# Performance work log

Hardware: AMD Instinct MI355X
Metric: run time of the kernel (lower is better)

The kernel has to match this reference:

```python
import jax, jax.numpy as jnp
import numpy as np
import math

B, H, S, D = 4, 16, 2048, 64

def setup_inputs() -> dict:
    key = jax.random.key(0)
    kq, kk, kv, km = jax.random.split(key, 4)
    query = jax.random.normal(kq, (B, H, S, D), dtype=jnp.float32)
    k = jax.random.normal(kk, (B, H, S, D), dtype=jnp.float32)
    value = jax.random.normal(kv, (B, H, S, D), dtype=jnp.float32)
    mask = jax.random.randint(km, (1, 1, S, S), 0, 2) == 1  # True = masked
    return {"query": query, "key": k, "value": value, "mask": mask}

def reference(query, key, value, mask):
    # scores: [B,H,S,S]
    scale = 1.0 / math.sqrt(key.shape[-1])
    scores = jnp.einsum('bhqd,bhkd->bhqk', query, key) * scale
    scores = jnp.where(mask, -jnp.inf, scores)
    probs = jax.nn.softmax(scores, axis=-1)
    out = jnp.einsum('bhqk,bhkd->bhqd', probs, value)
    return out
```

## Files before the change

### kernel.cpp

```cpp
#include <hip/hip_runtime.h>
#include <hip/hip_bf16.h>
#include <stdint.h>

#define BHN 64
#define SEQ 2048
#define DH  64

typedef unsigned short u16;
typedef __attribute__((ext_vector_type(8))) short bf16x8;
typedef __attribute__((ext_vector_type(16))) float f32x16;

__device__ inline u16 f2bf(float x){
  union { float f; uint32_t u; } a; a.f = x;
  uint32_t u = a.u;
  uint32_t lsb = (u >> 16) & 1u;
  u += 0x7FFFu + lsb;
  return (u16)(u >> 16);
}

__device__ inline float fast_exp2(float x){
#if __has_builtin(__builtin_amdgcn_exp2f)
  return __builtin_amdgcn_exp2f(x);
#else
  float r; asm("v_exp_f32 %0, %1" : "=v"(r) : "v"(x)); return r;
#endif
}

__device__ inline void gload_lds16(const void* g, void* l){
  __builtin_amdgcn_global_load_lds(
      (const __attribute__((address_space(1))) void*)g,
      (__attribute__((address_space(3))) void*)l, 16, 0, 0);
}


__global__ __launch_bounds__(256) void build_tiles(const float* __restrict__ kf,
                                                   const float* __restrict__ vf,
                                                   u16* __restrict__ tiles){
  __shared__ float sVf[64][65];
  int head = blockIdx.x >> 5;
  int kt   = blockIdx.x & 31;
  int k0   = kt * 64;
  int t = threadIdx.x;

  {
    int r = t >> 2;
    int dseg = (t & 3) * 16;
    const float* src = vf + ((int64_t)(head*SEQ + k0 + r))*DH + dseg;
    #pragma unroll
    for (int j = 0; j < 16; j += 4){
      float4 v = *(const float4*)(src + j);
      sVf[r][dseg+j+0] = v.x; sVf[r][dseg+j+1] = v.y;
      sVf[r][dseg+j+2] = v.z; sVf[r][dseg+j+3] = v.w;
    }
  }

  u16* outb = tiles + ((size_t)(head*32 + kt) << 13);

  #pragma unroll
  for (int i = 0; i < 2; i++){
    int cid = i*256 + t;
    int f = cid >> 6;
    int l = cid & 63;
    int kh = f >> 2, ds = f & 3;
    int row = k0 + kh*32 + (l & 31);
    int dstart = ds*16 + (l >> 5)*8;
    const float* src = kf + ((int64_t)(head*SEQ + row))*DH + dstart;
    float4 a = *(const float4*)(src);
    float4 b = *(const float4*)(src + 4);
    union { u16 h[8]; uint4 v; } pk;
    pk.h[0]=f2bf(a.x); pk.h[1]=f2bf(a.y); pk.h[2]=f2bf(a.z); pk.h[3]=f2bf(a.w);
    pk.h[4]=f2bf(b.x); pk.h[5]=f2bf(b.y); pk.h[6]=f2bf(b.z); pk.h[7]=f2bf(b.w);
    *(uint4*)(outb + f*512 + l*8) = pk.v;
  }

  __syncthreads();

  #pragma unroll
  for (int i = 0; i < 2; i++){
    int cid = i*256 + t;
    int g = cid >> 6;
    int l = cid & 63;
    int oh = g >> 2, ks = g & 3;
    int d  = oh*32 + (l & 31);
    int kk = ks*16 + (l >> 5)*8;
    union { u16 h[8]; uint4 v; } pk;
    #pragma unroll
    for (int j = 0; j < 8; j++) pk.h[j] = f2bf(sVf[kk+j][d]);
    *(uint4*)(outb + (8+g)*512 + l*8) = pk.v;
  }
}

__global__ __launch_bounds__(256) void pack_mask(const void* __restrict__ mraw,
                                                 uint32_t* __restrict__ mkp){
  __shared__ int sflag;
  int t = threadIdx.x;
  const uint32_t* m32 = (const uint32_t*)mraw;
  if (t == 0) sflag = 0;
  __syncthreads();
  if (t < 64){
    uint32_t v = m32[t] | m32[t+64] | m32[t+128] | m32[t+192];
    if (v > 1u) atomicOr(&sflag, 1);
  }
  __syncthreads();
  bool isbool = (sflag != 0);
  int idx = blockIdx.x*256 + t;
  int row = idx >> 6;
  int wd  = idx & 63;
  uint32_t bits = 0;
  if (isbool){
    const uint8_t* mb = (const uint8_t*)mraw + (int64_t)row*SEQ + wd*32;
    uint4 a = ((const uint4*)mb)[0];
    uint4 b = ((const uint4*)mb)[1];
    uint32_t words[8] = {a.x,a.y,a.z,a.w,b.x,b.y,b.z,b.w};
    #pragma unroll
    for (int i = 0; i < 32; i++){
      int kl = (i&3) + 8*((i>>2)&3) + 4*(i>>4);
      uint32_t byte = (words[kl>>2] >> (8*(kl&3))) & 0xFFu;
      bits |= (byte ? 0u : 1u) << i;
    }
  } else {
    const uint32_t* mi = m32 + (int64_t)row*SEQ + wd*32;
    uint32_t words[32];
    #pragma unroll
    for (int j = 0; j < 32; j += 4){
      uint4 v = *(const uint4*)(mi + j);
      words[j+0]=v.x; words[j+1]=v.y; words[j+2]=v.z; words[j+3]=v.w;
    }
    #pragma unroll
    for (int i = 0; i < 32; i++){
      int kl = (i&3) + 8*((i>>2)&3) + 4*(i>>4);
      bits |= (words[kl] ? 0u : 1u) << i;
    }
  }
  mkp[((size_t)(wd >> 2)*SEQ + row)*4 + (wd & 3)] = bits;
}


__global__ __launch_bounds__(512, 4) void attn_mfma(
    const float* __restrict__ qf, const u16* __restrict__ tiles,
    const uint32_t* __restrict__ mkp, float* __restrict__ out)
{
  __shared__ __align__(16) char lds[2*32768 + 1024];

  int bid = blockIdx.x;
  int logical = (bid & 7)*64 + (bid >> 3);
  int head = logical >> 3;
  int q0   = (logical & 7) * 256;

  int t  = threadIdx.x;
  int w  = t >> 6;
  int l  = t & 63;
  int l31 = l & 31;
  int hi  = l >> 5;
  int hi16 = hi << 4;

  const float QS = 0.125f * 1.4426950408889634f;
  bf16x8 qfr[4];
  {
    const float* qrow = qf + ((size_t)(head*SEQ + q0 + w*32 + l31))*DH + hi*8;
    #pragma unroll
    for (int ds = 0; ds < 4; ds++){
      float4 a = *(const float4*)(qrow + ds*16);
      float4 b = *(const float4*)(qrow + ds*16 + 4);
      uint32_t u0, u1, u2, u3;
      asm("v_cvt_pk_bf16_f32 %0, %1, %2" : "=v"(u0) : "v"(a.x*QS), "v"(a.y*QS));
      asm("v_cvt_pk_bf16_f32 %0, %1, %2" : "=v"(u1) : "v"(a.z*QS), "v"(a.w*QS));
      asm("v_cvt_pk_bf16_f32 %0, %1, %2" : "=v"(u2) : "v"(b.x*QS), "v"(b.y*QS));
      asm("v_cvt_pk_bf16_f32 %0, %1, %2" : "=v"(u3) : "v"(b.z*QS), "v"(b.w*QS));
      union { uint32_t u[4]; bf16x8 h; } pk_;
      pk_.u[0]=u0; pk_.u[1]=u1; pk_.u[2]=u2; pk_.u[3]=u3;
      qfr[ds] = pk_.h;
    }
  }

  const uint4* mbase = (const uint4*)mkp + (q0 + w*32 + l31);

  const char* tb = (const char*)tiles + ((size_t)head << 19) + w*4096 + l*16;
  char* dwave = lds + w*4096;

  f32x16 O0 = {0,0,0,0,0,0,0,0,0,0,0,0,0,0,0,0};
  f32x16 O1 = {0,0,0,0,0,0,0,0,0,0,0,0,0,0,0,0};
  float ls0 = 0.f, ls1 = 0.f;

  const char* ldsL = lds + l*16;

  auto STAGE = [&](int kt128, int bufoff){
    const char* s_ = tb + ((size_t)kt128 << 15);
    char* d_ = dwave + bufoff;
    gload_lds16(s_,        d_);
    gload_lds16(s_ + 1024, d_ + 1024);
    gload_lds16(s_ + 2048, d_ + 2048);
    gload_lds16(s_ + 3072, d_ + 3072);
  };

  auto SMPACK = [&](f32x16& c, bf16x8& pa0, bf16x8& pa1){
    float p[16];
    #pragma unroll
    for (int r = 0; r < 16; r++) p[r] = fast_exp2(c[r]);
    #pragma unroll
    for (int r = 0; r < 8; r++){ ls0 += p[r]; ls1 += p[r+8]; }
    {
      uint32_t A0, A1, B0, B1;
      asm("v_cvt_pk_bf16_f32 %0, %1, %2" : "=v"(A0) : "v"(p[0]), "v"(p[1]));
      asm("v_cvt_pk_bf16_f32 %0, %1, %2" : "=v"(A1) : "v"(p[2]), "v"(p[3]));
      asm("v_cvt_pk_bf16_f32 %0, %1, %2" : "=v"(B0) : "v"(p[4]), "v"(p[5]));
      asm("v_cvt_pk_bf16_f32 %0, %1, %2" : "=v"(B1) : "v"(p[6]), "v"(p[7]));
      asm("v_permlane32_swap_b32 %0, %1" : "+v"(A0), "+v"(B0));
      asm("v_permlane32_swap_b32 %0, %1" : "+v"(A1), "+v"(B1));
      union { uint32_t u[4]; bf16x8 h; } pk_;
      pk_.u[0] = A0; pk_.u[1] = A1; pk_.u[2] = B0; pk_.u[3] = B1;
      pa0 = pk_.h;
    }
    {
      uint32_t A0, A1, B0, B1;
      asm("v_cvt_pk_bf16_f32 %0, %1, %2" : "=v"(A0) : "v"(p[8]),  "v"(p[9]));
      asm("v_cvt_pk_bf16_f32 %0, %1, %2" : "=v"(A1) : "v"(p[10]), "v"(p[11]));
      asm("v_cvt_pk_bf16_f32 %0, %1, %2" : "=v"(B0) : "v"(p[12]), "v"(p[13]));
      asm("v_cvt_pk_bf16_f32 %0, %1, %2" : "=v"(B1) : "v"(p[14]), "v"(p[15]));
      asm("v_permlane32_swap_b32 %0, %1" : "+v"(A0), "+v"(B0));
      asm("v_permlane32_swap_b32 %0, %1" : "+v"(A1), "+v"(B1));
      union { uint32_t u[4]; bf16x8 h; } pk_;
      pk_.u[0] = A0; pk_.u[1] = A1; pk_.u[2] = B0; pk_.u[3] = B1;
      pa1 = pk_.h;
    }
  };

  STAGE(0, 0);
  asm volatile("" ::: "memory");
  uint4 mw4 = *mbase;

  int cur = 0;
  #pragma unroll 1
  for (int kt = 0; kt < 16; kt++){
    int nt = (kt < 15) ? (kt + 1) : 15;
    STAGE(nt, cur ^ 32768);
    asm volatile("" ::: "memory");
    uint4 mnext = mbase[(size_t)nt*SEQ];

    asm volatile("s_waitcnt vmcnt(5)" ::: "memory");
    __builtin_amdgcn_s_barrier();
    asm volatile("" ::: "memory");

    uint32_t mm[4] = {mw4.x, mw4.y, mw4.z, mw4.w};

    #pragma unroll
    for (int h = 0; h < 2; h++){
      const char* lb = ldsL + cur + h*16384;
      uint32_t nsh0 = ~(mm[2*h]   >> hi16);
      uint32_t nsh1 = ~(mm[2*h+1] >> hi16);

      f32x16 c0, c1;
      #pragma unroll
      for (int r = 0; r < 16; r++){
        int32_t km;
        asm("v_bfe_i32 %0, %1, %2, 1" : "=v"(km) : "v"(nsh0), "n"(r));
        c0[r] = __uint_as_float((uint32_t)km & 0xC3000000u);
      }
      #pragma unroll
      for (int r = 0; r < 16; r++){
        int32_t km;
        asm("v_bfe_i32 %0, %1, %2, 1" : "=v"(km) : "v"(nsh1), "n"(r));
        c1[r] = __uint_as_float((uint32_t)km & 0xC3000000u);
      }

      __builtin_amdgcn_s_setprio(1);
      #pragma unroll
      for (int ds = 0; ds < 4; ds++){
        bf16x8 kfr = *(const bf16x8*)(lb + ds*1024);
        c0 = __builtin_amdgcn_mfma_f32_32x32x16_bf16(kfr, qfr[ds], c0, 0, 0, 0);
      }
      #pragma unroll
      for (int ds = 0; ds < 4; ds++){
        bf16x8 kfr = *(const bf16x8*)(lb + (4 + ds)*1024);
        c1 = __builtin_amdgcn_mfma_f32_32x32x16_bf16(kfr, qfr[ds], c1, 0, 0, 0);
      }
      __builtin_amdgcn_s_setprio(0);

      bf16x8 pa0, pa1;
      SMPACK(c0, pa0, pa1);

      __builtin_amdgcn_s_setprio(1);
      {
        bf16x8 v00 = *(const bf16x8*)(lb + 8*1024);
        bf16x8 v01 = *(const bf16x8*)(lb + 9*1024);
        bf16x8 v10 = *(const bf16x8*)(lb + 12*1024);
        bf16x8 v11 = *(const bf16x8*)(lb + 13*1024);
        O0 = __builtin_amdgcn_mfma_f32_32x32x16_bf16(pa0, v00, O0, 0, 0, 0);
        O0 = __builtin_amdgcn_mfma_f32_32x32x16_bf16(pa1, v01, O0, 0, 0, 0);
        O1 = __builtin_amdgcn_mfma_f32_32x32x16_bf16(pa0, v10, O1, 0, 0, 0);
        O1 = __builtin_amdgcn_mfma_f32_32x32x16_bf16(pa1, v11, O1, 0, 0, 0);
      }
      __builtin_amdgcn_s_setprio(0);

      bf16x8 pb0, pb1;
      SMPACK(c1, pb0, pb1);

      __builtin_amdgcn_s_setprio(1);
      {
        bf16x8 v00 = *(const bf16x8*)(lb + 10*1024);
        bf16x8 v01 = *(const bf16x8*)(lb + 11*1024);
        bf16x8 v10 = *(const bf16x8*)(lb + 14*1024);
        bf16x8 v11 = *(const bf16x8*)(lb + 15*1024);
        O0 = __builtin_amdgcn_mfma_f32_32x32x16_bf16(pb0, v00, O0, 0, 0, 0);
        O0 = __builtin_amdgcn_mfma_f32_32x32x16_bf16(pb1, v01, O0, 0, 0, 0);
        O1 = __builtin_amdgcn_mfma_f32_32x32x16_bf16(pb0, v10, O1, 0, 0, 0);
        O1 = __builtin_amdgcn_mfma_f32_32x32x16_bf16(pb1, v11, O1, 0, 0, 0);
      }
      __builtin_amdgcn_s_setprio(0);
    }

    asm volatile("" ::: "memory");
    __builtin_amdgcn_s_barrier();
    asm volatile("" ::: "memory");

    mw4 = mnext;
    cur ^= 32768;
  }

  float lt = ls0 + ls1;
  {
    uint32_t a = __float_as_uint(lt), b = a;
    asm("v_permlane32_swap_b32 %0, %1" : "+v"(a), "+v"(b));
    lt = __uint_as_float(a) + __uint_as_float(b);
  }
  float* sInv = (float*)(lds + 65536);
  if (hi == 0) sInv[w*32 + l31] = 1.0f / lt;
  float* obase = out + ((size_t)(head*SEQ + q0 + w*32))*DH + l31;
  #pragma unroll
  for (int r = 0; r < 16; r++){
    int qr = (r&3) + 8*(r>>2) + 4*hi;
    float inv = sInv[w*32 + qr];
    obase[(size_t)qr*DH]      = O0[r] * inv;
    obase[(size_t)qr*DH + 32] = O1[r] * inv;
  }
}


__global__ __launch_bounds__(256) void attn_naive(
    const float* __restrict__ qf, const float* __restrict__ kf,
    const float* __restrict__ vf, const void* __restrict__ mraw,
    float* __restrict__ out)
{
  __shared__ float sq[64];
  __shared__ float sS[SEQ];
  __shared__ float redM[4], redS[4];
  __shared__ float sO[4][64];
  __shared__ int sflag;

  int bid = blockIdx.x;
  int bh = bid >> 11;
  int q  = bid & 2047;
  int t  = threadIdx.x;
  const uint32_t* m32 = (const uint32_t*)mraw;
  if (t == 0) sflag = 0;
  __syncthreads();
  if (t < 64){
    uint32_t v = m32[t] | m32[t+64] | m32[t+128] | m32[t+192];
    if (v > 1u) atomicOr(&sflag, 1);
  }
  if (t < 64) sq[t] = qf[((int64_t)bh*SEQ + q)*DH + t] * (0.125f*1.4426950408889634f);
  __syncthreads();
  bool isbool = (sflag != 0);

  float lmax = -3e38f;
  for (int k = t; k < SEQ; k += 256){
    bool masked = isbool ? (((const uint8_t*)mraw)[(int64_t)q*SEQ + k] != 0)
                         : (m32[(int64_t)q*SEQ + k] != 0);
    float s = -3e38f;
    if (!masked){
      const float* krow = kf + ((int64_t)bh*SEQ + k)*DH;
      float acc = 0.f;
      for (int d = 0; d < 64; d++) acc += sq[d]*krow[d];
      s = acc;
    }
    sS[k] = s;
    lmax = fmaxf(lmax, s);
  }
  for (int o = 32; o >= 1; o >>= 1) lmax = fmaxf(lmax, __shfl_xor(lmax, o));
  if ((t & 63) == 0) redM[t >> 6] = lmax;
  __syncthreads();
  float m = fmaxf(fmaxf(redM[0], redM[1]), fmaxf(redM[2], redM[3]));
  float lsum = 0.f;
  for (int k = t; k < SEQ; k += 256){
    float p = exp2f(sS[k] - m);
    sS[k] = p;
    lsum += p;
  }
  for (int o = 32; o >= 1; o >>= 1) lsum += __shfl_xor(lsum, o);
  if ((t & 63) == 0) redS[t >> 6] = lsum;
  __syncthreads();
  float lden = redS[0] + redS[1] + redS[2] + redS[3];

  float o = 0.f;
  int d = t & 63;
  int c = t >> 6;
  for (int k = c*512; k < (c+1)*512; k++)
    o += sS[k] * vf[((int64_t)bh*SEQ + k)*DH + d];
  sO[c][d] = o;
  __syncthreads();
  if (t < 64){
    float r = (sO[0][t] + sO[1][t] + sO[2][t] + sO[3][t]) / lden;
    out[((int64_t)bh*SEQ + q)*DH + t] = r;
  }
}


extern "C" void kernel_launch(void* const* d_in, const int* in_sizes, int n_in,
                              void* d_out, int out_size, void* d_ws, size_t ws_size,
                              hipStream_t stream)
{
  const float* qf = (const float*)d_in[0];
  const float* kf = (const float*)d_in[1];
  const float* vf = (const float*)d_in[2];
  const void*  mraw = d_in[3];
  float* out = (float*)d_out;

  size_t tilesB = (size_t)BHN*32*16384;
  size_t need = tilesB + (size_t)SEQ*64*4 + 256;
  if (ws_size >= need){
    u16* tiles = (u16*)d_ws;
    uint32_t* mkp = (uint32_t*)((char*)d_ws + tilesB);
    hipLaunchKernelGGL(build_tiles, dim3(2048), dim3(256), 0, stream, kf, vf, tiles);
    hipLaunchKernelGGL(pack_mask,   dim3(512),  dim3(256), 0, stream, mraw, mkp);
    hipLaunchKernelGGL(attn_mfma,   dim3(512),  dim3(512), 0, stream, qf, tiles, mkp, out);
  } else {
    hipLaunchKernelGGL(attn_naive, dim3(BHN*SEQ), dim3(256), 0, stream, qf, kf, vf, mraw, out);
  }
}
```

Before: 109.1 us.

## Merge tile build and mask pack into one prepass; rotate per-wave subtile order

The K/V tile conversion and mask bit-packing kernels are merged into a single prepass launch, with blocks beyond 2048 doing mask packing. This removes one kernel launch and lets the two independent prepasses overlap. In the attention loop, each wave now handles the four 32-key subtiles of a 128-key block in a rotated order (offset by wave index) with one score accumulator at a time. The mask words are permuted to match the rotation. This staggers LDS access and MFMA/exp phases across waves and cuts register pressure, at the cost of extra select logic per iteration.

After: 113.0 us. +3.6%, slower.

```diff
diff --git a/kernel.cpp b/kernel.cpp
--- a/kernel.cpp
+++ b/kernel.cpp
@@ -33,106 +33,106 @@
 }
 
 
-__global__ __launch_bounds__(256) void build_tiles(const float* __restrict__ kf,
-                                                   const float* __restrict__ vf,
-                                                   u16* __restrict__ tiles){
-  __shared__ float sVf[64][65];
-  int head = blockIdx.x >> 5;
-  int kt   = blockIdx.x & 31;
-  int k0   = kt * 64;
+__global__ __launch_bounds__(256) void prepass(const float* __restrict__ kf,
+                                               const float* __restrict__ vf,
+                                               const void* __restrict__ mraw,
+                                               u16* __restrict__ tiles,
+                                               uint32_t* __restrict__ mkp){
   int t = threadIdx.x;
-
-  {
-    int r = t >> 2;
-    int dseg = (t & 3) * 16;
-    const float* src = vf + ((int64_t)(head*SEQ + k0 + r))*DH + dseg;
+  if (blockIdx.x < 2048){
+    __shared__ float sVf[64][65];
+    int head = blockIdx.x >> 5;
+    int kt   = blockIdx.x & 31;
+    int k0   = kt * 64;
+
+    {
+      int r = t >> 2;
+      int dseg = (t & 3) * 16;
+      const float* src = vf + ((int64_t)(head*SEQ + k0 + r))*DH + dseg;
+      #pragma unroll
+      for (int j = 0; j < 16; j += 4){
+        float4 v = *(const float4*)(src + j);
+        sVf[r][dseg+j+0] = v.x; sVf[r][dseg+j+1] = v.y;
+        sVf[r][dseg+j+2] = v.z; sVf[r][dseg+j+3] = v.w;
+      }
+    }
+
+    u16* outb = tiles + ((size_t)(head*32 + kt) << 13);
+
     #pragma unroll
-    for (int j = 0; j < 16; j += 4){
-      float4 v = *(const float4*)(src + j);
-      sVf[r][dseg+j+0] = v.x; sVf[r][dseg+j+1] = v.y;
-      sVf[r][dseg+j+2] = v.z; sVf[r][dseg+j+3] = v.w;
-    }
-  }
-
-  u16* outb = tiles + ((size_t)(head*32 + kt) << 13);
-
-  #pragma unroll
-  for (int i = 0; i < 2; i++){
-    int cid = i*256 + t;
-    int f = cid >> 6;
-    int l = cid & 63;
-    int kh = f >> 2, ds = f & 3;
-    int row = k0 + kh*32 + (l & 31);
-    int dstart = ds*16 + (l >> 5)*8;
-    const float* src = kf + ((int64_t)(head*SEQ + row))*DH + dstart;
-    float4 a = *(const float4*)(src);
-    float4 b = *(const float4*)(src + 4);
-    union { u16 h[8]; uint4 v; } pk;
-    pk.h[0]=f2bf(a.x); pk.h[1]=f2bf(a.y); pk.h[2]=f2bf(a.z); pk.h[3]=f2bf(a.w);
-    pk.h[4]=f2bf(b.x); pk.h[5]=f2bf(b.y); pk.h[6]=f2bf(b.z); pk.h[7]=f2bf(b.w);
-    *(uint4*)(outb + f*512 + l*8) = pk.v;
-  }
-
-  __syncthreads();
-
-  #pragma unroll
-  for (int i = 0; i < 2; i++){
-    int cid = i*256 + t;
-    int g = cid >> 6;
-    int l = cid & 63;
-    int oh = g >> 2, ks = g & 3;
-    int d  = oh*32 + (l & 31);
-    int kk = ks*16 + (l >> 5)*8;
-    union { u16 h[8]; uint4 v; } pk;
+    for (int i = 0; i < 2; i++){
+      int cid = i*256 + t;
+      int f = cid >> 6;
+      int l = cid & 63;
+      int kh = f >> 2, ds = f & 3;
+      int row = k0 + kh*32 + (l & 31);
+      int dstart = ds*16 + (l >> 5)*8;
+      const float* src = kf + ((int64_t)(head*SEQ + row))*DH + dstart;
+      float4 a = *(const float4*)(src);
+      float4 b = *(const float4*)(src + 4);
+      union { u16 h[8]; uint4 v; } pk;
+      pk.h[0]=f2bf(a.x); pk.h[1]=f2bf(a.y); pk.h[2]=f2bf(a.z); pk.h[3]=f2bf(a.w);
+      pk.h[4]=f2bf(b.x); pk.h[5]=f2bf(b.y); pk.h[6]=f2bf(b.z); pk.h[7]=f2bf(b.w);
+      *(uint4*)(outb + f*512 + l*8) = pk.v;
+    }
+
+    __syncthreads();
+
     #pragma unroll
-    for (int j = 0; j < 8; j++) pk.h[j] = f2bf(sVf[kk+j][d]);
-    *(uint4*)(outb + (8+g)*512 + l*8) = pk.v;
-  }
-}
-
-__global__ __launch_bounds__(256) void pack_mask(const void* __restrict__ mraw,
-                                                 uint32_t* __restrict__ mkp){
-  __shared__ int sflag;
-  int t = threadIdx.x;
-  const uint32_t* m32 = (const uint32_t*)mraw;
-  if (t == 0) sflag = 0;
-  __syncthreads();
-  if (t < 64){
-    uint32_t v = m32[t] | m32[t+64] | m32[t+128] | m32[t+192];
-    if (v > 1u) atomicOr(&sflag, 1);
-  }
-  __syncthreads();
-  bool isbool = (sflag != 0);
-  int idx = blockIdx.x*256 + t;
-  int row = idx >> 6;
-  int wd  = idx & 63;
-  uint32_t bits = 0;
-  if (isbool){
-    const uint8_t* mb = (const uint8_t*)mraw + (int64_t)row*SEQ + wd*32;
-    uint4 a = ((const uint4*)mb)[0];
-    uint4 b = ((const uint4*)mb)[1];
-    uint32_t words[8] = {a.x,a.y,a.z,a.w,b.x,b.y,b.z,b.w};
-    #pragma unroll
-    for (int i = 0; i < 32; i++){
-      int kl = (i&3) + 8*((i>>2)&3) + 4*(i>>4);
-      uint32_t byte = (words[kl>>2] >> (8*(kl&3))) & 0xFFu;
-      bits |= (byte ? 0u : 1u) << i;
+    for (int i = 0; i < 2; i++){
+      int cid = i*256 + t;
+      int g = cid >> 6;
+      int l = cid & 63;
+      int oh = g >> 2, ks = g & 3;
+      int d  = oh*32 + (l & 31);
+      int kk = ks*16 + (l >> 5)*8;
+      union { u16 h[8]; uint4 v; } pk;
+      #pragma unroll
+      for (int j = 0; j < 8; j++) pk.h[j] = f2bf(sVf[kk+j][d]);
+      *(uint4*)(outb + (8+g)*512 + l*8) = pk.v;
     }
   } else {
-    const uint32_t* mi = m32 + (int64_t)row*SEQ + wd*32;
-    uint32_t words[32];
-    #pragma unroll
-    for (int j = 0; j < 32; j += 4){
-      uint4 v = *(const uint4*)(mi + j);
-      words[j+0]=v.x; words[j+1]=v.y; words[j+2]=v.z; words[j+3]=v.w;
-    }
-    #pragma unroll
-    for (int i = 0; i < 32; i++){
-      int kl = (i&3) + 8*((i>>2)&3) + 4*(i>>4);
-      bits |= (words[kl] ? 0u : 1u) << i;
-    }
-  }
-  mkp[((size_t)(wd >> 2)*SEQ + row)*4 + (wd & 3)] = bits;
+    __shared__ int sflag;
+    const uint32_t* m32 = (const uint32_t*)mraw;
+    if (t == 0) sflag = 0;
+    __syncthreads();
+    if (t < 64){
+      uint32_t v = m32[t] | m32[t+64] | m32[t+128] | m32[t+192];
+      if (v > 1u) atomicOr(&sflag, 1);
+    }
+    __syncthreads();
+    bool isbool = (sflag != 0);
+    int idx = (blockIdx.x - 2048)*256 + t;
+    int row = idx >> 6;
+    int wd  = idx & 63;
+    uint32_t bits = 0;
+    if (isbool){
+      const uint8_t* mb = (const uint8_t*)mraw + (int64_t)row*SEQ + wd*32;
+      uint4 a = ((const uint4*)mb)[0];
+      uint4 b = ((const uint4*)mb)[1];
+      uint32_t words[8] = {a.x,a.y,a.z,a.w,b.x,b.y,b.z,b.w};
+      #pragma unroll
+      for (int i = 0; i < 32; i++){
+        int kl = (i&3) + 8*((i>>2)&3) + 4*(i>>4);
+        uint32_t byte = (words[kl>>2] >> (8*(kl&3))) & 0xFFu;
+        bits |= (byte ? 0u : 1u) << i;
+      }
+    } else {
+      const uint32_t* mi = m32 + (int64_t)row*SEQ + wd*32;
+      uint32_t words[32];
+      #pragma unroll
+      for (int j = 0; j < 32; j += 4){
+        uint4 v = *(const uint4*)(mi + j);
+        words[j+0]=v.x; words[j+1]=v.y; words[j+2]=v.z; words[j+3]=v.w;
+      }
+      #pragma unroll
+      for (int i = 0; i < 32; i++){
+        int kl = (i&3) + 8*((i>>2)&3) + 4*(i>>4);
+        bits |= (words[kl] ? 0u : 1u) << i;
+      }
+    }
+    mkp[((size_t)(wd >> 2)*SEQ + row)*4 + (wd & 3)] = bits;
+  }
 }
 
 
@@ -153,6 +153,7 @@
   int l31 = l & 31;
   int hi  = l >> 5;
   int hi16 = hi << 4;
+  int wrot = w & 3;
 
   const float QS = 0.125f * 1.4426950408889634f;
   bf16x8 qfr[4];
@@ -193,38 +194,6 @@
     gload_lds16(s_ + 3072, d_ + 3072);
   };
 
-  auto SMPACK = [&](f32x16& c, bf16x8& pa0, bf16x8& pa1){
-    float p[16];
-    #pragma unroll
-    for (int r = 0; r < 16; r++) p[r] = fast_exp2(c[r]);
-    #pragma unroll
-    for (int r = 0; r < 8; r++){ ls0 += p[r]; ls1 += p[r+8]; }
-    {
-      uint32_t A0, A1, B0, B1;
-      asm("v_cvt_pk_bf16_f32 %0, %1, %2" : "=v"(A0) : "v"(p[0]), "v"(p[1]));
-      asm("v_cvt_pk_bf16_f32 %0, %1, %2" : "=v"(A1) : "v"(p[2]), "v"(p[3]));
-      asm("v_cvt_pk_bf16_f32 %0, %1, %2" : "=v"(B0) : "v"(p[4]), "v"(p[5]));
-      asm("v_cvt_pk_bf16_f32 %0, %1, %2" : "=v"(B1) : "v"(p[6]), "v"(p[7]));
-      asm("v_permlane32_swap_b32 %0, %1" : "+v"(A0), "+v"(B0));
-      asm("v_permlane32_swap_b32 %0, %1" : "+v"(A1), "+v"(B1));
-      union { uint32_t u[4]; bf16x8 h; } pk_;
-      pk_.u[0] = A0; pk_.u[1] = A1; pk_.u[2] = B0; pk_.u[3] = B1;
-      pa0 = pk_.h;
-    }
-    {
-      uint32_t A0, A1, B0, B1;
-      asm("v_cvt_pk_bf16_f32 %0, %1, %2" : "=v"(A0) : "v"(p[8]),  "v"(p[9]));
-      asm("v_cvt_pk_bf16_f32 %0, %1, %2" : "=v"(A1) : "v"(p[10]), "v"(p[11]));
-      asm("v_cvt_pk_bf16_f32 %0, %1, %2" : "=v"(B0) : "v"(p[12]), "v"(p[13]));
-      asm("v_cvt_pk_bf16_f32 %0, %1, %2" : "=v"(B1) : "v"(p[14]), "v"(p[15]));
-      asm("v_permlane32_swap_b32 %0, %1" : "+v"(A0), "+v"(B0));
-      asm("v_permlane32_swap_b32 %0, %1" : "+v"(A1), "+v"(B1));
-      union { uint32_t u[4]; bf16x8 h; } pk_;
-      pk_.u[0] = A0; pk_.u[1] = A1; pk_.u[2] = B0; pk_.u[3] = B1;
-      pa1 = pk_.h;
-    }
-  };
-
   STAGE(0, 0);
   asm volatile("" ::: "memory");
   uint4 mw4 = *mbase;
@@ -241,70 +210,87 @@
     __builtin_amdgcn_s_barrier();
     asm volatile("" ::: "memory");
 
-    uint32_t mm[4] = {mw4.x, mw4.y, mw4.z, mw4.w};
+    uint32_t a0 = mw4.x, a1 = mw4.y, a2 = mw4.z, a3 = mw4.w;
+    uint32_t b0, b1, b2, b3;
+    {
+      uint32_t c0 = (wrot & 1) ? a1 : a0;
+      uint32_t c1 = (wrot & 1) ? a2 : a1;
+      uint32_t c2 = (wrot & 1) ? a3 : a2;
+      uint32_t c3 = (wrot & 1) ? a0 : a3;
+      b0 = (wrot & 2) ? c2 : c0;
+      b1 = (wrot & 2) ? c3 : c1;
+      b2 = (wrot & 2) ? c0 : c2;
+      b3 = (wrot & 2) ? c1 : c3;
+    }
+    uint32_t bm[4]; bm[0]=b0; bm[1]=b1; bm[2]=b2; bm[3]=b3;
 
     #pragma unroll
-    for (int h = 0; h < 2; h++){
-      const char* lb = ldsL + cur + h*16384;
-      uint32_t nsh0 = ~(mm[2*h]   >> hi16);
-      uint32_t nsh1 = ~(mm[2*h+1] >> hi16);
-
-      f32x16 c0, c1;
+    for (int gi = 0; gi < 4; gi++){
+      int g2 = (gi + wrot) & 3;
+      int hh = g2 >> 1;
+      int gg = g2 & 1;
+      const char* lbK = ldsL + cur + hh*16384 + gg*4096;
+      const char* lbV = ldsL + cur + hh*16384 + 8192 + gg*2048;
+      uint32_t nsh = ~(bm[gi] >> hi16);
+
+      f32x16 c;
       #pragma unroll
       for (int r = 0; r < 16; r++){
         int32_t km;
-        asm("v_bfe_i32 %0, %1, %2, 1" : "=v"(km) : "v"(nsh0), "n"(r));
-        c0[r] = __uint_as_float((uint32_t)km & 0xC3000000u);
-      }
-      #pragma unroll
-      for (int r = 0; r < 16; r++){
-        int32_t km;
-        asm("v_bfe_i32 %0, %1, %2, 1" : "=v"(km) : "v"(nsh1), "n"(r));
-        c1[r] = __uint_as_float((uint32_t)km & 0xC3000000u);
+        asm("v_bfe_i32 %0, %1, %2, 1" : "=v"(km) : "v"(nsh), "n"(r));
+        c[r] = __uint_as_float((uint32_t)km & 0xC3000000u);
       }
 
       __builtin_amdgcn_s_setprio(1);
       #pragma unroll
       for (int ds = 0; ds < 4; ds++){
-        bf16x8 kfr = *(const bf16x8*)(lb + ds*1024);
-        c0 = __builtin_amdgcn_mfma_f32_32x32x16_bf16(kfr, qfr[ds], c0, 0, 0, 0);
-      }
-      #pragma unroll
-      for (int ds = 0; ds < 4; ds++){
-        bf16x8 kfr = *(const bf16x8*)(lb + (4 + ds)*1024);
-        c1 = __builtin_amdgcn_mfma_f32_32x32x16_bf16(kfr, qfr[ds], c1, 0, 0, 0);
+        bf16x8 kfr = *(const bf16x8*)(lbK + ds*1024);
+        c = __builtin_amdgcn_mfma_f32_32x32x16_bf16(kfr, qfr[ds], c, 0, 0, 0);
       }
       __builtin_amdgcn_s_setprio(0);
 
+      float p[16];
+      #pragma unroll
+      for (int r = 0; r < 16; r++) p[r] = fast_exp2(c[r]);
+      #pragma unroll
+      for (int r = 0; r < 8; r++){ ls0 += p[r]; ls1 += p[r+8]; }
+
       bf16x8 pa0, pa1;
-      SMPACK(c0, pa0, pa1);
+      {
+        uint32_t A0, A1, B0, B1;
+        asm("v_cvt_pk_bf16_f32 %0, %1, %2" : "=v"(A0) : "v"(p[0]), "v"(p[1]));
+        asm("v_cvt_pk_bf16_f32 %0, %1, %2" : "=v"(A1) : "v"(p[2]), "v"(p[3]));
+        asm("v_cvt_pk_bf16_f32 %0, %1, %2" : "=v"(B0) : "v"(p[4]), "v"(p[5]));
+        asm("v_cvt_pk_bf16_f32 %0, %1, %2" : "=v"(B1) : "v"(p[6]), "v"(p[7]));
+        asm("v_permlane32_swap_b32 %0, %1" : "+v"(A0), "+v"(B0));
+        asm("v_permlane32_swap_b32 %0, %1" : "+v"(A1), "+v"(B1));
+        union { uint32_t u[4]; bf16x8 h; } pk_;
+        pk_.u[0] = A0; pk_.u[1] = A1; pk_.u[2] = B0; pk_.u[3] = B1;
+        pa0 = pk_.h;
+      }
+      {
+        uint32_t A0, A1, B0, B1;
+        asm("v_cvt_pk_bf16_f32 %0, %1, %2" : "=v"(A0) : "v"(p[8]),  "v"(p[9]));
+        asm("v_cvt_pk_bf16_f32 %0, %1, %2" : "=v"(A1) : "v"(p[10]), "v"(p[11]));
+        asm("v_cvt_pk_bf16_f32 %0, %1, %2" : "=v"(B0) : "v"(p[12]), "v"(p[13]));
+        asm("v_cvt_pk_bf16_f32 %0, %1, %2" : "=v"(B1) : "v"(p[14]), "v"(p[15]));
+        asm("v_permlane32_swap_b32 %0, %1" : "+v"(A0), "+v"(B0));
+        asm("v_permlane32_swap_b32 %0, %1" : "+v"(A1), "+v"(B1));
+        union { uint32_t u[4]; bf16x8 h; } pk_;
+        pk_.u[0] = A0; pk_.u[1] = A1; pk_.u[2] = B0; pk_.u[3] = B1;
+        pa1 = pk_.h;
+      }
 
       __builtin_amdgcn_s_setprio(1);
       {
-        bf16x8 v00 = *(const bf16x8*)(lb + 8*1024);
-        bf16x8 v01 = *(const bf16x8*)(lb + 9*1024);
-        bf16x8 v10 = *(const bf16x8*)(lb + 12*1024);
-        bf16x8 v11 = *(const bf16x8*)(lb + 13*1024);
+        bf16x8 v00 = *(const bf16x8*)(lbV);
+        bf16x8 v01 = *(const bf16x8*)(lbV + 1024);
+        bf16x8 v10 = *(const bf16x8*)(lbV + 4096);
+        bf16x8 v11 = *(const bf16x8*)(lbV + 5120);
         O0 = __builtin_amdgcn_mfma_f32_32x32x16_bf16(pa0, v00, O0, 0, 0, 0);
         O0 = __builtin_amdgcn_mfma_f32_32x32x16_bf16(pa1, v01, O0, 0, 0, 0);
         O1 = __builtin_amdgcn_mfma_f32_32x32x16_bf16(pa0, v10, O1, 0, 0, 0);
         O1 = __builtin_amdgcn_mfma_f32_32x32x16_bf16(pa1, v11, O1, 0, 0, 0);
-      }
-      __builtin_amdgcn_s_setprio(0);
-
-      bf16x8 pb0, pb1;
-      SMPACK(c1, pb0, pb1);
-
-      __builtin_amdgcn_s_setprio(1);
-      {
-        bf16x8 v00 = *(const bf16x8*)(lb + 10*1024);
-        bf16x8 v01 = *(const bf16x8*)(lb + 11*1024);
-        bf16x8 v10 = *(const bf16x8*)(lb + 14*1024);
-        bf16x8 v11 = *(const bf16x8*)(lb + 15*1024);
-        O0 = __builtin_amdgcn_mfma_f32_32x32x16_bf16(pb0, v00, O0, 0, 0, 0);
-        O0 = __builtin_amdgcn_mfma_f32_32x32x16_bf16(pb1, v01, O0, 0, 0, 0);
-        O1 = __builtin_amdgcn_mfma_f32_32x32x16_bf16(pb0, v10, O1, 0, 0, 0);
-        O1 = __builtin_amdgcn_mfma_f32_32x32x16_bf16(pb1, v11, O1, 0, 0, 0);
       }
       __builtin_amdgcn_s_setprio(0);
     }
@@ -420,9 +406,8 @@
   if (ws_size >= need){
     u16* tiles = (u16*)d_ws;
     uint32_t* mkp = (uint32_t*)((char*)d_ws + tilesB);
-    hipLaunchKernelGGL(build_tiles, dim3(2048), dim3(256), 0, stream, kf, vf, tiles);
-    hipLaunchKernelGGL(pack_mask,   dim3(512),  dim3(256), 0, stream, mraw, mkp);
-    hipLaunchKernelGGL(attn_mfma,   dim3(512),  dim3(512), 0, stream, qf, tiles, mkp, out);
+    hipLaunchKernelGGL(prepass,   dim3(2560), dim3(256), 0, stream, kf, vf, mraw, tiles, mkp);
+    hipLaunchKernelGGL(attn_mfma, dim3(512),  dim3(512), 0, stream, qf, tiles, mkp, out);
   } else {
     hipLaunchKernelGGL(attn_naive, dim3(BHN*SEQ), dim3(256), 0, stream, qf, kf, vf, mraw, out);
   }
```
